# Kernel optimization log

Hardware: AMD Instinct MI355X
Metric: run time of the kernel (lower is better)

The kernel has to match this reference:

```python
import jax, jax.numpy as jnp
import numpy as np

B, T, H, N = 4, 2048, 512, 8
THETA = 10000.0
PERIOD, RET_ORDER = 3, 2  # num_inputs, mgdt ret_order


def setup_inputs() -> dict:
    key = jax.random.key(0)
    ks = jax.random.split(key, 9)
    s = 0.02
    return {
        "x": jax.random.normal(ks[0], (B, T, H), dtype=jnp.float32),
        "Wq": jax.random.normal(ks[1], (H, H), dtype=jnp.float32) * s,
        "bq": jax.random.normal(ks[2], (H,), dtype=jnp.float32) * s,
        "Wk": jax.random.normal(ks[3], (H, H), dtype=jnp.float32) * s,
        "bk": jax.random.normal(ks[4], (H,), dtype=jnp.float32) * s,
        "Wv": jax.random.normal(ks[5], (H, H), dtype=jnp.float32) * s,
        "bv": jax.random.normal(ks[6], (H,), dtype=jnp.float32) * s,
        "Wo": jax.random.normal(ks[7], (H, H), dtype=jnp.float32) * s,
        "bo": jax.random.normal(ks[8], (H,), dtype=jnp.float32) * s,
    }


def _rope(z, cos, sin):
    # RoPE over the FULL hidden dim (applied before head split, as in source)
    b, t, c = z.shape
    z = z.reshape(b, t, c // 2, 2)
    zr = z[..., 0] * cos - z[..., 1] * sin
    zi = z[..., 0] * sin + z[..., 1] * cos
    return jnp.stack([zr, zi], axis=-1).reshape(b, t, c)


def reference(x, Wq, bq, Wk, bk, Wv, bv, Wo, bo):
    Bx, Tx, C = x.shape
    D = C // N

    # precomputed freqs_cis -> cos/sin, shape (T, C//2)
    inv_freq = 1.0 / (THETA ** (jnp.arange(0, C, 2, dtype=jnp.float32) / C))
    ang = jnp.arange(Tx, dtype=jnp.float32)[:, None] * inv_freq[None, :]
    cos, sin = jnp.cos(ang), jnp.sin(ang)

    q = x @ Wq + bq
    k = x @ Wk + bk
    q = _rope(q, cos, sin)
    k = _rope(k, cos, sin)
    v = x @ Wv + bv

    # (B, N, T, D)
    q = q.reshape(Bx, Tx, N, D).transpose(0, 2, 1, 3)
    k = k.reshape(Bx, Tx, N, D).transpose(0, 2, 1, 3)
    v = v.reshape(Bx, Tx, N, D).transpose(0, 2, 1, 3)

    scores = jnp.einsum("bntd,bnsd->bnts", q, k) / jnp.float32(D) ** 0.5

    # causal tril mask with mgdt column masking (cols period+ret_order-1, step period)
    mask = jnp.tril(jnp.ones((Tx, Tx), dtype=bool))
    ret_cols = np.arange(PERIOD + RET_ORDER - 1, Tx, PERIOD)
    mask = mask.at[:, ret_cols].set(False)

    scores = jnp.where(mask[None, None], scores, -jnp.inf)
    att = jax.nn.softmax(scores, axis=-1)  # (B,N,T,T)

    out = jnp.einsum("bnts,bnsd->bntd", att, v)
    out = out.transpose(0, 2, 1, 3).reshape(Bx, Tx, C)
    return out @ Wo + bo
```

## Files before the change

### kernel.cpp

```cpp
#include <hip/hip_runtime.h>

typedef unsigned short u16;
typedef __attribute__((ext_vector_type(8))) short bf16x8;
typedef __attribute__((ext_vector_type(8))) unsigned short u16x8;
typedef __attribute__((ext_vector_type(4))) float f32x4;
typedef __attribute__((ext_vector_type(16))) float f32x16;
typedef __attribute__((ext_vector_type(4))) unsigned int u32x4;

#define MFMA16(a, b, c) __builtin_amdgcn_mfma_f32_16x16x32_bf16((a), (b), (c), 0, 0, 0)
#define MFMA32(a, b, c) __builtin_amdgcn_mfma_f32_32x32x16_bf16((a), (b), (c), 0, 0, 0)

static constexpr int CB = 4, CT = 2048, CH = 512, CN = 8, CD = 64;
static constexpr int CM = CB * CT;

__device__ __forceinline__ u16 f2bf(float f) {
    union { float f; unsigned int i; } v; v.f = f;
    unsigned int r = v.i + 0x7FFFu + ((v.i >> 16) & 1u);
    return (u16)(r >> 16);
}

__device__ __forceinline__ int kc_of(int t) {
    return t + 1 - ((t >= 4) ? ((t - 1) / 3) : 0);
}

__device__ __forceinline__ void gl16(const u16* g, u16* l) {
    __builtin_amdgcn_global_load_lds(
        (const __attribute__((address_space(1))) void*)g,
        (__attribute__((address_space(3))) void*)l, 16, 0, 0);
}


__global__ void cvt_x_kernel(const float* __restrict__ x, u16* __restrict__ xb, int n4) {
    int i = blockIdx.x * blockDim.x + threadIdx.x;
    const float4* x4 = (const float4*)x;
    for (; i < n4; i += gridDim.x * blockDim.x) {
        float4 v = x4[i];
        unsigned long long pack = (unsigned long long)f2bf(v.x)
                                | ((unsigned long long)f2bf(v.y) << 16)
                                | ((unsigned long long)f2bf(v.z) << 32)
                                | ((unsigned long long)f2bf(v.w) << 48);
        ((unsigned long long*)xb)[i] = pack;
    }
}

__global__ void wt_kernel(const float* __restrict__ Wq, const float* __restrict__ Wk,
                          const float* __restrict__ Wv, const float* __restrict__ Wo,
                          u16* __restrict__ Wt) {
    __shared__ float tile[32][33];
    const float* W = (blockIdx.z == 0) ? Wq : (blockIdx.z == 1) ? Wk
                   : (blockIdx.z == 2) ? Wv : Wo;
    u16* dst = Wt + (size_t)blockIdx.z * CH * CH;
    int n0 = blockIdx.x * 32, k0 = blockIdx.y * 32;
    int tx = threadIdx.x, ty = threadIdx.y;
    for (int j = 0; j < 32; j += 8)
        tile[ty + j][tx] = W[(size_t)(k0 + ty + j) * CH + n0 + tx];
    __syncthreads();
    for (int j = 0; j < 32; j += 8)
        dst[(size_t)(n0 + ty + j) * CH + k0 + tx] = f2bf(tile[tx][ty + j]);
}

__global__ void rope_tab_kernel(float2* __restrict__ tab) {
    int i = blockIdx.x * blockDim.x + threadIdx.x;
    if (i >= CT * (CH / 2)) return;
    int t = i >> 8, h = i & 255;
    float inv = exp2f(-(float)h * (13.287712379549449f / 256.0f));
    float ang = (float)t * inv;
    float s, c;
    sincosf(ang, &s, &c);
    tab[i] = make_float2(c, s);
}


__device__ __forceinline__ void gemm_bt_main(const u16* __restrict__ A, const u16* __restrict__ Bt,
                                             int m0, int n0, f32x4 acc[4][2]) {
    __shared__ __align__(16) u16 Al[128 * 32];
    __shared__ __align__(16) u16 Bl[128 * 32];
    const int tid = threadIdx.x;
    const int lane = tid & 63;
    const int w = tid >> 6;
    const int wm = w >> 2, wn = w & 3;
    const int lg = lane >> 4, lr = lane & 15;

    const int srow = w * 16 + (lane >> 2);
    const int schunk = ((lane & 3) ^ ((lane >> 3) & 3)) * 8;
    const u16* ga = A  + (size_t)(m0 + srow) * CH + schunk;
    const u16* gb = Bt + (size_t)(n0 + srow) * CH + schunk;
    u16* lA0 = Al + w * 512;
    u16* lB0 = Bl + w * 512;

    const int rchunk = (lg ^ ((lr >> 1) & 3)) * 8;

    for (int k0 = 0; k0 < CH; k0 += 32) {
        __syncthreads();
        gl16(ga + k0, lA0);
        gl16(gb + k0, lB0);
        __syncthreads();
        bf16x8 af[4], bfr[2];
#pragma unroll
        for (int i = 0; i < 4; ++i)
            af[i] = *(const bf16x8*)(Al + (wm * 64 + i * 16 + lr) * 32 + rchunk);
#pragma unroll
        for (int i = 0; i < 2; ++i)
            bfr[i] = *(const bf16x8*)(Bl + (wn * 32 + i * 16 + lr) * 32 + rchunk);
#pragma unroll
        for (int mi = 0; mi < 4; ++mi)
#pragma unroll
            for (int ni = 0; ni < 2; ++ni)
                acc[mi][ni] = MFMA16(af[mi], bfr[ni], acc[mi][ni]);
    }
}

__global__ __launch_bounds__(512) void gemm_qkv_kernel(
    const u16* __restrict__ xb, const u16* __restrict__ Wt,
    const float* __restrict__ bq, const float* __restrict__ bk, const float* __restrict__ bv,
    const float2* __restrict__ tab,
    u16* __restrict__ q_ws, u16* __restrict__ k_ws, u16* __restrict__ v_t) {
    f32x4 acc[4][2];
#pragma unroll
    for (int mi = 0; mi < 4; ++mi)
#pragma unroll
        for (int ni = 0; ni < 2; ++ni)
#pragma unroll
            for (int e = 0; e < 4; ++e) acc[mi][ni][e] = 0.f;

    const int m0 = blockIdx.x * 128, n0 = blockIdx.y * 128;
    gemm_bt_main(xb, Wt, m0, n0, acc);

    const int lane = threadIdx.x & 63;
    const int w = threadIdx.x >> 6, wm = w >> 2, wn = w & 3;
    const int lg = lane >> 4, lr = lane & 15;
    const int seg = n0 >> 9;
    const float* bias_p = (seg == 0) ? bq : (seg == 1) ? bk : bv;

#pragma unroll
    for (int ni = 0; ni < 2; ++ni) {
        const int c = n0 + wn * 32 + ni * 16 + lr;
        const int cc = c & 511;
        const int nh = cc >> 6, d = cc & 63;
        const float bias = bias_p[cc];
#pragma unroll
        for (int mi = 0; mi < 4; ++mi) {
#pragma unroll
            for (int r = 0; r < 4; ++r) {
                const int row = m0 + wm * 64 + mi * 16 + lg * 4 + r;
                const int b = row >> 11, t = row & 2047;
                float val = acc[mi][ni][r] + bias;
                if (seg < 2) {
                    float2 cs = tab[t * 256 + (cc >> 1)];
                    float partner = __shfl_xor(val, 1);
                    val = val * cs.x + ((lane & 1) ? partner * cs.y : -partner * cs.y);
                }
                if (seg == 0) {
                    val *= 0.18033688011112f;
                    q_ws[(size_t)((b * CN + nh) * CT + t) * CD + d] = f2bf(val);
                } else {
                    const bool msk = (t >= 4) && (t % 3 == 1);
                    if (!msk) {
                        const int ci = t - ((t >= 4) ? ((t - 1) / 3) : 0);
                        const int tile = ci >> 5, sl = ci & 31;
                        const size_t tb = (size_t)(b * CN + nh) * CT * CD + (size_t)tile * 2048;
                        if (seg == 1) {
                            const int cF = d >> 4, hF = (d >> 3) & 1, jF = d & 7;
                            k_ws[tb + ((cF * 2 + hF) * 32 + sl) * 8 + jF] = f2bf(val);
                        } else {
                            const int kbF = sl >> 4, hF = (sl >> 3) & 1, jF = sl & 7;
                            const int dhF = d >> 5, qlF = d & 31;
                            v_t[tb + (((dhF * 2 + kbF) * 2 + hF) * 32 + qlF) * 8 + jF] = f2bf(val);
                        }
                    }
                }
            }
        }
    }
}


__global__ __launch_bounds__(512) void gemm_out_kernel(
    const u16* __restrict__ att, const u16* __restrict__ Wot,
    const float* __restrict__ bo, float* __restrict__ out) {
    __shared__ __align__(16) u16 Al[64 * 32];
    __shared__ __align__(16) u16 Bl[128 * 32];
    f32x4 acc[2][2];
#pragma unroll
    for (int mi = 0; mi < 2; ++mi)
#pragma unroll
        for (int ni = 0; ni < 2; ++ni)
#pragma unroll
            for (int e = 0; e < 4; ++e) acc[mi][ni][e] = 0.f;

    const int m0 = blockIdx.x * 64, n0 = blockIdx.y * 128;
    const int tid = threadIdx.x;
    const int lane = tid & 63;
    const int w = tid >> 6;
    const int wm = w >> 2, wn = w & 3;
    const int lg = lane >> 4, lr = lane & 15;

    const int srow = lane >> 2;
    const int schunk = ((lane & 3) ^ ((lane >> 3) & 3)) * 8;
    const u16* ga = att + (size_t)(m0 + w * 16 + srow) * CH + schunk;
    const u16* gb = Wot + (size_t)(n0 + w * 16 + srow) * CH + schunk;
    const int rchunk = (lg ^ ((lr >> 1) & 3)) * 8;

    for (int k0 = 0; k0 < CH; k0 += 32) {
        __syncthreads();
        if (w < 4) gl16(ga + k0, Al + w * 512);
        gl16(gb + k0, Bl + w * 512);
        __syncthreads();
        bf16x8 af[2], bfr[2];
#pragma unroll
        for (int i = 0; i < 2; ++i) {
            af[i]  = *(const bf16x8*)(Al + (wm * 32 + i * 16 + lr) * 32 + rchunk);
            bfr[i] = *(const bf16x8*)(Bl + (wn * 32 + i * 16 + lr) * 32 + rchunk);
        }
#pragma unroll
        for (int mi = 0; mi < 2; ++mi)
#pragma unroll
            for (int ni = 0; ni < 2; ++ni)
                acc[mi][ni] = MFMA16(af[mi], bfr[ni], acc[mi][ni]);
    }

#pragma unroll
    for (int ni = 0; ni < 2; ++ni) {
        const int c = n0 + wn * 32 + ni * 16 + lr;
        const float bias = bo[c];
#pragma unroll
        for (int mi = 0; mi < 2; ++mi)
#pragma unroll
            for (int r = 0; r < 4; ++r) {
                const int row = m0 + wm * 32 + mi * 16 + lg * 4 + r;
                out[(size_t)row * CH + c] = acc[mi][ni][r] + bias;
            }
    }
}

__global__ __launch_bounds__(256, 4) void attn_kernel(
    const u16* __restrict__ q_ws, const u16* __restrict__ k_ws,
    const u16* __restrict__ v_t, u16* __restrict__ attout) {
    const int bid = blockIdx.x;
    const int xcd = bid & 7, idx = bid >> 3;
    const int bn = xcd + 8 * (idx >> 6);
    const int qb = 63 - (idx & 63);
    const int q0 = qb * 32;
    const int l = threadIdx.x & 63;
    const int w = threadIdx.x >> 6;
    const int ql = l & 31, h = l >> 5;

    const int t = q0 + ql;
    const int kct = kc_of(t);
    const int kcq0 = kc_of(q0);
    const int kcmax = kc_of(q0 + 31);
    const int ntc32 = (kcmax + 31) >> 5;

    const size_t baseq = (size_t)bn * CT * CD;
    const size_t basek = (size_t)bn * CT * CD;
    const size_t basev = (size_t)bn * CD * CT;

    bf16x8 qf[4];
    {
        const u16* qp = q_ws + baseq + (size_t)t * CD + h * 8;
#pragma unroll
        for (int c = 0; c < 4; ++c) qf[c] = *(const bf16x8*)(qp + c * 16);
    }

    f32x16 oa[2];
#pragma unroll
    for (int dh = 0; dh < 2; ++dh)
#pragma unroll
        for (int e = 0; e < 16; ++e) oa[dh][e] = 0.f;
    float lsum = 0.f;

    for (int i32 = w; i32 < ntc32; i32 += 4) {
        const int s0h = i32 * 32;
        const bool needmask = (s0h + 31 >= kcq0);
        const u16* ktile = k_ws + basek + (size_t)i32 * 2048;
        const u16* vtile = v_t + basev + (size_t)i32 * 2048;

        f32x16 sa;
#pragma unroll
        for (int e = 0; e < 16; ++e) sa[e] = 0.f;
#pragma unroll
        for (int c = 0; c < 4; ++c) {
            bf16x8 kf = *(const bf16x8*)(ktile + ((c * 2 + h) * 32 + ql) * 8);
            sa = MFMA32(kf, qf[c], sa);
        }

        float pr[16];
        if (needmask) {
#pragma unroll
            for (int g = 0; g < 16; ++g) {
                const int roff = (g & 3) + 8 * (g >> 2);
                float e = __builtin_amdgcn_exp2f(sa[g]);
                e = (s0h + roff + 4 * h < kct) ? e : 0.f;
                lsum += e;
                pr[g] = e;
            }
        } else {
#pragma unroll
            for (int g = 0; g < 16; ++g) {
                float e = __builtin_amdgcn_exp2f(sa[g]);
                lsum += e;
                pr[g] = e;
            }
        }

#pragma unroll
        for (int kb = 0; kb < 2; ++kb) {
            const int g0 = kb * 8;
            unsigned int w0, w1, w2, w3;
            asm("v_cvt_pk_bf16_f32 %0, %1, %2" : "=v"(w0) : "v"(pr[g0 + 0]), "v"(pr[g0 + 1]));
            asm("v_cvt_pk_bf16_f32 %0, %1, %2" : "=v"(w1) : "v"(pr[g0 + 2]), "v"(pr[g0 + 3]));
            asm("v_cvt_pk_bf16_f32 %0, %1, %2" : "=v"(w2) : "v"(pr[g0 + 4]), "v"(pr[g0 + 5]));
            asm("v_cvt_pk_bf16_f32 %0, %1, %2" : "=v"(w3) : "v"(pr[g0 + 6]), "v"(pr[g0 + 7]));
            const unsigned int x0 = (unsigned int)__shfl_xor((int)w0, 32);
            const unsigned int x1 = (unsigned int)__shfl_xor((int)w1, 32);
            const unsigned int x2 = (unsigned int)__shfl_xor((int)w2, 32);
            const unsigned int x3 = (unsigned int)__shfl_xor((int)w3, 32);
            u32x4 fw;
            fw.x = h ? x2 : w0;
            fw.y = h ? x3 : w1;
            fw.z = h ? w2 : x0;
            fw.w = h ? w3 : x1;
            const bf16x8 pa = __builtin_bit_cast(bf16x8, fw);
#pragma unroll
            for (int dh = 0; dh < 2; ++dh) {
                bf16x8 vf = *(const bf16x8*)(vtile + (((dh * 2 + kb) * 2 + h) * 32 + ql) * 8);
                oa[dh] = MFMA32(pa, vf, oa[dh]);
            }
        }
    }

    __shared__ float buf[2][64][33];
    __shared__ float lsp[4][64];
    __shared__ float lsf[32];

    lsp[w][l] = lsum;
    if (w >= 2) {
#pragma unroll
        for (int dh = 0; dh < 2; ++dh)
#pragma unroll
            for (int g = 0; g < 16; ++g)
                buf[w - 2][l][dh * 16 + g] = oa[dh][g];
    }
    __syncthreads();
    if (w < 2) {
#pragma unroll
        for (int dh = 0; dh < 2; ++dh)
#pragma unroll
            for (int g = 0; g < 16; ++g)
                oa[dh][g] += buf[w][l][dh * 16 + g];
    }
    if (threadIdx.x < 32) {
        const int r = threadIdx.x;
        float s = 0.f;
#pragma unroll
        for (int ww = 0; ww < 4; ++ww) s += lsp[ww][r] + lsp[ww][r + 32];
        lsf[r] = 1.f / s;
    }
    __syncthreads();
    if (w == 1) {
#pragma unroll
        for (int dh = 0; dh < 2; ++dh)
#pragma unroll
            for (int g = 0; g < 16; ++g)
                buf[0][l][dh * 16 + g] = oa[dh][g];
    }
    __syncthreads();
    if (w == 0) {
        const int b = bn >> 3, nh = bn & 7;
#pragma unroll
        for (int dh = 0; dh < 2; ++dh)
#pragma unroll
            for (int g = 0; g < 16; ++g) {
                const float s = oa[dh][g] + buf[0][l][dh * 16 + g];
                const int r = (g & 3) + 8 * (g >> 2) + 4 * h;
                attout[(size_t)(b * CT + q0 + r) * CH + nh * 64 + dh * 32 + ql] = f2bf(s * lsf[r]);
            }
    }
}


extern "C" void kernel_launch(void* const* d_in, const int* in_sizes, int n_in,
                              void* d_out, int out_size, void* d_ws, size_t ws_size,
                              hipStream_t stream) {
    const float* x  = (const float*)d_in[0];
    const float* Wq = (const float*)d_in[1];
    const float* bq = (const float*)d_in[2];
    const float* Wk = (const float*)d_in[3];
    const float* bk = (const float*)d_in[4];
    const float* Wv = (const float*)d_in[5];
    const float* bv = (const float*)d_in[6];
    const float* Wo = (const float*)d_in[7];
    const float* bo = (const float*)d_in[8];
    float* out = (float*)d_out;

    char* p = (char*)d_ws;
    u16* xb = (u16*)p;        p += (size_t)CM * CH * 2;
    u16* Wt = (u16*)p;        p += (size_t)4 * CH * CH * 2;
    float2* tab = (float2*)p; p += (size_t)CT * (CH / 2) * 8;
    u16* q_ws = (u16*)p;      p += (size_t)CM * CH * 2;
    u16* k_ws = (u16*)p;      p += (size_t)CM * CH * 2;
    u16* v_t  = (u16*)p;      p += (size_t)CM * CH * 2;
    u16* attout = (u16*)p;    p += (size_t)CM * CH * 2;

    cvt_x_kernel<<<2048, 256, 0, stream>>>(x, xb, CM * CH / 4);
    wt_kernel<<<dim3(16, 16, 4), dim3(32, 8), 0, stream>>>(Wq, Wk, Wv, Wo, Wt);
    rope_tab_kernel<<<dim3((CT * (CH / 2)) / 256), 256, 0, stream>>>(tab);
    gemm_qkv_kernel<<<dim3(CM / 128, (3 * CH) / 128), 512, 0, stream>>>(
        xb, Wt, bq, bk, bv, tab, q_ws, k_ws, v_t);
    attn_kernel<<<dim3(2048), 256, 0, stream>>>(q_ws, k_ws, v_t, attout);
    gemm_out_kernel<<<dim3(CM / 64, CH / 128), 512, 0, stream>>>(
        attout, Wt + (size_t)3 * CH * CH, bo, out);
}
```

Baseline: 83.65 us.

## Merge prep kernels into one launch and retile QKV GEMM to 128x96

Fuses the x-to-bf16 conversion, weight transpose and RoPE table kernels into a single prep kernel that dispatches on block index, removing two launches and their serialization gaps. The QKV GEMM tile changes from 128x128 to 128x96 with a 4x2 wave layout, giving each wave 2x3 MFMA tiles and 16 column blocks instead of 12, for more blocks and better CU occupancy. The segment (q/k/v) is now computed per column, since a 96-wide tile can straddle a segment boundary. In exchange each block reuses its A tile less, and two waves idle during B loads.

```diff
diff --git a/kernel.cpp b/kernel.cpp
--- a/kernel.cpp
+++ b/kernel.cpp
@@ -29,83 +29,79 @@
         (__attribute__((address_space(3))) void*)l, 16, 0, 0);
 }
 
-
-__global__ void cvt_x_kernel(const float* __restrict__ x, u16* __restrict__ xb, int n4) {
-    int i = blockIdx.x * blockDim.x + threadIdx.x;
-    const float4* x4 = (const float4*)x;
-    for (; i < n4; i += gridDim.x * blockDim.x) {
-        float4 v = x4[i];
-        unsigned long long pack = (unsigned long long)f2bf(v.x)
-                                | ((unsigned long long)f2bf(v.y) << 16)
-                                | ((unsigned long long)f2bf(v.z) << 32)
-                                | ((unsigned long long)f2bf(v.w) << 48);
-        ((unsigned long long*)xb)[i] = pack;
-    }
-}
-
-__global__ void wt_kernel(const float* __restrict__ Wq, const float* __restrict__ Wk,
-                          const float* __restrict__ Wv, const float* __restrict__ Wo,
-                          u16* __restrict__ Wt) {
-    __shared__ float tile[32][33];
-    const float* W = (blockIdx.z == 0) ? Wq : (blockIdx.z == 1) ? Wk
-                   : (blockIdx.z == 2) ? Wv : Wo;
-    u16* dst = Wt + (size_t)blockIdx.z * CH * CH;
-    int n0 = blockIdx.x * 32, k0 = blockIdx.y * 32;
-    int tx = threadIdx.x, ty = threadIdx.y;
-    for (int j = 0; j < 32; j += 8)
-        tile[ty + j][tx] = W[(size_t)(k0 + ty + j) * CH + n0 + tx];
-    __syncthreads();
-    for (int j = 0; j < 32; j += 8)
-        dst[(size_t)(n0 + ty + j) * CH + k0 + tx] = f2bf(tile[tx][ty + j]);
-}
-
-__global__ void rope_tab_kernel(float2* __restrict__ tab) {
-    int i = blockIdx.x * blockDim.x + threadIdx.x;
-    if (i >= CT * (CH / 2)) return;
-    int t = i >> 8, h = i & 255;
-    float inv = exp2f(-(float)h * (13.287712379549449f / 256.0f));
-    float ang = (float)t * inv;
-    float s, c;
-    sincosf(ang, &s, &c);
-    tab[i] = make_float2(c, s);
-}
-
-
-__device__ __forceinline__ void gemm_bt_main(const u16* __restrict__ A, const u16* __restrict__ Bt,
-                                             int m0, int n0, f32x4 acc[4][2]) {
+__global__ __launch_bounds__(256) void prep_kernel(
+    const float* __restrict__ x, u16* __restrict__ xb,
+    const float* __restrict__ Wq, const float* __restrict__ Wk,
+    const float* __restrict__ Wv, const float* __restrict__ Wo,
+    u16* __restrict__ Wt, float2* __restrict__ tab) {
+    const int blk = blockIdx.x;
+    if (blk < 1024) {
+        __shared__ float tile[32][33];
+        const int z = blk >> 8, rem = blk & 255;
+        const int n0 = (rem & 15) * 32, k0 = (rem >> 4) * 32;
+        const float* W = (z == 0) ? Wq : (z == 1) ? Wk : (z == 2) ? Wv : Wo;
+        u16* dst = Wt + (size_t)z * CH * CH;
+        const int tx = threadIdx.x & 31, ty = threadIdx.x >> 5;
+        for (int j = 0; j < 32; j += 8)
+            tile[ty + j][tx] = W[(size_t)(k0 + ty + j) * CH + n0 + tx];
+        __syncthreads();
+        for (int j = 0; j < 32; j += 8)
+            dst[(size_t)(n0 + ty + j) * CH + k0 + tx] = f2bf(tile[tx][ty + j]);
+    } else if (blk < 3072) {
+        const int i = (blk - 1024) * 256 + threadIdx.x;
+        const int t = i >> 8, h = i & 255;
+        float inv = exp2f(-(float)h * (13.287712379549449f / 256.0f));
+        float s, c;
+        sincosf((float)t * inv, &s, &c);
+        tab[i] = make_float2(c, s);
+    } else {
+        const int n4 = CM * CH / 4;
+        const float4* x4 = (const float4*)x;
+        for (int i = (blk - 3072) * 256 + threadIdx.x; i < n4; i += 2048 * 256) {
+            float4 v = x4[i];
+            unsigned long long pack = (unsigned long long)f2bf(v.x)
+                                    | ((unsigned long long)f2bf(v.y) << 16)
+                                    | ((unsigned long long)f2bf(v.z) << 32)
+                                    | ((unsigned long long)f2bf(v.w) << 48);
+            ((unsigned long long*)xb)[i] = pack;
+        }
+    }
+}
+
+
+__device__ __forceinline__ void gemm_bt_qkv(const u16* __restrict__ A, const u16* __restrict__ Bt,
+                                            int m0, int n0, f32x4 acc[2][3]) {
     __shared__ __align__(16) u16 Al[128 * 32];
-    __shared__ __align__(16) u16 Bl[128 * 32];
+    __shared__ __align__(16) u16 Bl[96 * 32];
     const int tid = threadIdx.x;
     const int lane = tid & 63;
     const int w = tid >> 6;
-    const int wm = w >> 2, wn = w & 3;
+    const int wm = w >> 1, wn = w & 1;
     const int lg = lane >> 4, lr = lane & 15;
 
-    const int srow = w * 16 + (lane >> 2);
+    const int srow = lane >> 2;
     const int schunk = ((lane & 3) ^ ((lane >> 3) & 3)) * 8;
-    const u16* ga = A  + (size_t)(m0 + srow) * CH + schunk;
-    const u16* gb = Bt + (size_t)(n0 + srow) * CH + schunk;
-    u16* lA0 = Al + w * 512;
-    u16* lB0 = Bl + w * 512;
+    const u16* ga = A  + (size_t)(m0 + w * 16 + srow) * CH + schunk;
+    const u16* gb = Bt + (size_t)(n0 + w * 16 + srow) * CH + schunk;
 
     const int rchunk = (lg ^ ((lr >> 1) & 3)) * 8;
 
     for (int k0 = 0; k0 < CH; k0 += 32) {
         __syncthreads();
-        gl16(ga + k0, lA0);
-        gl16(gb + k0, lB0);
+        gl16(ga + k0, Al + w * 512);
+        if (w < 6) gl16(gb + k0, Bl + w * 512);
         __syncthreads();
-        bf16x8 af[4], bfr[2];
-#pragma unroll
-        for (int i = 0; i < 4; ++i)
-            af[i] = *(const bf16x8*)(Al + (wm * 64 + i * 16 + lr) * 32 + rchunk);
+        bf16x8 af[2], bfr[3];
 #pragma unroll
         for (int i = 0; i < 2; ++i)
-            bfr[i] = *(const bf16x8*)(Bl + (wn * 32 + i * 16 + lr) * 32 + rchunk);
-#pragma unroll
-        for (int mi = 0; mi < 4; ++mi)
-#pragma unroll
-            for (int ni = 0; ni < 2; ++ni)
+            af[i] = *(const bf16x8*)(Al + (wm * 32 + i * 16 + lr) * 32 + rchunk);
+#pragma unroll
+        for (int j = 0; j < 3; ++j)
+            bfr[j] = *(const bf16x8*)(Bl + (wn * 48 + j * 16 + lr) * 32 + rchunk);
+#pragma unroll
+        for (int mi = 0; mi < 2; ++mi)
+#pragma unroll
+            for (int ni = 0; ni < 3; ++ni)
                 acc[mi][ni] = MFMA16(af[mi], bfr[ni], acc[mi][ni]);
     }
 }
@@ -115,34 +111,34 @@
     const float* __restrict__ bq, const float* __restrict__ bk, const float* __restrict__ bv,
     const float2* __restrict__ tab,
     u16* __restrict__ q_ws, u16* __restrict__ k_ws, u16* __restrict__ v_t) {
-    f32x4 acc[4][2];
-#pragma unroll
-    for (int mi = 0; mi < 4; ++mi)
-#pragma unroll
-        for (int ni = 0; ni < 2; ++ni)
+    f32x4 acc[2][3];
+#pragma unroll
+    for (int mi = 0; mi < 2; ++mi)
+#pragma unroll
+        for (int ni = 0; ni < 3; ++ni)
 #pragma unroll
             for (int e = 0; e < 4; ++e) acc[mi][ni][e] = 0.f;
 
-    const int m0 = blockIdx.x * 128, n0 = blockIdx.y * 128;
-    gemm_bt_main(xb, Wt, m0, n0, acc);
+    const int m0 = blockIdx.x * 128, n0 = blockIdx.y * 96;
+    gemm_bt_qkv(xb, Wt, m0, n0, acc);
 
     const int lane = threadIdx.x & 63;
-    const int w = threadIdx.x >> 6, wm = w >> 2, wn = w & 3;
+    const int w = threadIdx.x >> 6, wm = w >> 1, wn = w & 1;
     const int lg = lane >> 4, lr = lane & 15;
-    const int seg = n0 >> 9;
-    const float* bias_p = (seg == 0) ? bq : (seg == 1) ? bk : bv;
-
-#pragma unroll
-    for (int ni = 0; ni < 2; ++ni) {
-        const int c = n0 + wn * 32 + ni * 16 + lr;
+
+#pragma unroll
+    for (int ni = 0; ni < 3; ++ni) {
+        const int c = n0 + wn * 48 + ni * 16 + lr;
+        const int seg = c >> 9;
         const int cc = c & 511;
         const int nh = cc >> 6, d = cc & 63;
+        const float* bias_p = (seg == 0) ? bq : (seg == 1) ? bk : bv;
         const float bias = bias_p[cc];
 #pragma unroll
-        for (int mi = 0; mi < 4; ++mi) {
+        for (int mi = 0; mi < 2; ++mi) {
 #pragma unroll
             for (int r = 0; r < 4; ++r) {
-                const int row = m0 + wm * 64 + mi * 16 + lg * 4 + r;
+                const int row = m0 + wm * 32 + mi * 16 + lg * 4 + r;
                 const int b = row >> 11, t = row & 2047;
                 float val = acc[mi][ni][r] + bias;
                 if (seg < 2) {
@@ -402,10 +398,8 @@
     u16* v_t  = (u16*)p;      p += (size_t)CM * CH * 2;
     u16* attout = (u16*)p;    p += (size_t)CM * CH * 2;
 
-    cvt_x_kernel<<<2048, 256, 0, stream>>>(x, xb, CM * CH / 4);
-    wt_kernel<<<dim3(16, 16, 4), dim3(32, 8), 0, stream>>>(Wq, Wk, Wv, Wo, Wt);
-    rope_tab_kernel<<<dim3((CT * (CH / 2)) / 256), 256, 0, stream>>>(tab);
-    gemm_qkv_kernel<<<dim3(CM / 128, (3 * CH) / 128), 512, 0, stream>>>(
+    prep_kernel<<<dim3(5120), 256, 0, stream>>>(x, xb, Wq, Wk, Wv, Wo, Wt, tab);
+    gemm_qkv_kernel<<<dim3(CM / 128, (3 * CH) / 96), 512, 0, stream>>>(
         xb, Wt, bq, bk, bv, tab, q_ws, k_ws, v_t);
     attn_kernel<<<dim3(2048), 256, 0, stream>>>(q_ws, k_ws, v_t, attout);
     gemm_out_kernel<<<dim3(CM / 64, CH / 128), 512, 0, stream>>>(
```

Measured after the change: 86.08 us. 1.03x slower.
